# Kernel tuning notes

Measured on AMD Instinct MI355X. Metric: run time of the kernel, lower is better.

## Reference

```python
import jax, jax.numpy as jnp
import numpy as np

N, E, F, ED, H, L, O = 100000, 600000, 64, 16, 128, 4, 32


def _ln(x, g, b, eps=1e-5):
    mu = jnp.mean(x, axis=-1, keepdims=True)
    var = jnp.mean((x - mu) ** 2, axis=-1, keepdims=True)
    return (x - mu) / jnp.sqrt(var + eps) * g + b


def setup_inputs() -> dict:
    key = jax.random.key(0)
    ks = iter(jax.random.split(key, 40))
    s = 0.05
    rn = lambda *shape: jax.random.normal(next(ks), shape, dtype=jnp.float32) * s
    inp = {
        'node_features': jax.random.normal(next(ks), (N, F), dtype=jnp.float32),
        'edge_index': jax.random.randint(next(ks), (2, E), 0, N, dtype=jnp.int64),
        'edge_features': jax.random.normal(next(ks), (E, ED), dtype=jnp.float32),
        # CircuitEncoder: Linear(F,H) -> ReLU -> LayerNorm(H) -> Linear(H,H) -> ReLU
        'enc_w1': rn(F, H), 'enc_b1': jnp.zeros((H,), jnp.float32),
        'enc_ln_g': jnp.ones((H,), jnp.float32), 'enc_ln_b': jnp.zeros((H,), jnp.float32),
        'enc_w2': rn(H, H), 'enc_b2': jnp.zeros((H,), jnp.float32),
        # L stacked GNN layers
        'msg_w1': rn(L, 2 * H + ED, H), 'msg_b1': jnp.zeros((L, H), jnp.float32),
        'msg_w2': rn(L, H, H), 'msg_b2': jnp.zeros((L, H), jnp.float32),
        'upd_w': rn(L, 2 * H, H), 'upd_b': jnp.zeros((L, H), jnp.float32),
        'ln_g': jnp.ones((L, H), jnp.float32), 'ln_b': jnp.zeros((L, H), jnp.float32),
        # GlobalAttentionPool: Linear(H,H//2) -> Tanh -> Linear(H//2,1)
        'att_w1': rn(H, H // 2), 'att_b1': jnp.zeros((H // 2,), jnp.float32),
        'att_w2': rn(H // 2, 1), 'att_b2': jnp.zeros((1,), jnp.float32),
        # output head (dropout is eval-mode identity)
        'head_w1': rn(H, H), 'head_b1': jnp.zeros((H,), jnp.float32),
        'head_w2': rn(H, O), 'head_b2': jnp.zeros((O,), jnp.float32),
    }
    return inp


def reference(node_features, edge_index, edge_features,
              enc_w1, enc_b1, enc_ln_g, enc_ln_b, enc_w2, enc_b2,
              msg_w1, msg_b1, msg_w2, msg_b2, upd_w, upd_b, ln_g, ln_b,
              att_w1, att_b1, att_w2, att_b2,
              head_w1, head_b1, head_w2, head_b2):
    # node encoder
    h = jax.nn.relu(node_features @ enc_w1 + enc_b1)
    h = _ln(h, enc_ln_g, enc_ln_b)
    h = jax.nn.relu(h @ enc_w2 + enc_b2)

    src, dst = edge_index[0], edge_index[1]
    ones_e = jnp.ones((E, 1), h.dtype)
    counts = jax.ops.segment_sum(ones_e, dst, num_segments=N)  # [N,1]
    inv_cnt = 1.0 / (counts + 1e-8)

    for i in range(L):
        # gather -> concat -> message MLP  [E, 2H+ED] -> [E, H]
        m_in = jnp.concatenate([h[src], h[dst], edge_features], axis=-1)
        m = jax.nn.relu(m_in @ msg_w1[i] + msg_b1[i]) @ msg_w2[i] + msg_b2[i]
        # scatter-mean aggregate
        agg = jax.ops.segment_sum(m, dst, num_segments=N) * inv_cnt
        h_new = jax.nn.relu(jnp.concatenate([h, agg], axis=-1) @ upd_w[i] + upd_b[i])
        h = _ln(h + h_new, ln_g[i], ln_b[i])

    # global attention pool (softmax over nodes, dim 0)
    scores = jnp.tanh(h @ att_w1 + att_b1) @ att_w2 + att_b2  # [N,1]
    attn = jax.nn.softmax(scores, axis=0)
    g = jnp.sum(attn * h, axis=0)  # [H]

    # output head (dropout = identity in eval)
    out = jax.nn.relu(g @ head_w1 + head_b1) @ head_w2 + head_b2  # [O]
    return out
```

## Files before the change

### kernel.cpp

```cpp
#include <hip/hip_runtime.h>
#include <hip/hip_bf16.h>

#define NN 100000
#define EE 600000
#define FF 64
#define EDIM 16
#define HH 128
#define LLAYERS 4
#define OO 32

#define SCH 512
#define SNB ((NN + SCH - 1) / SCH)


__global__ __launch_bounds__(64) void k_detect(const unsigned int* __restrict__ w,
                                               int* __restrict__ flag)
{
  const int t = threadIdx.x;
  int z = (w[2*t + 1] == 0u) ? 1 : 0;
  #pragma unroll
  for (int o = 32; o > 0; o >>= 1) z &= __shfl_xor(z, o, 64);
  if (t == 0) *flag = z;
}

__global__ __launch_bounds__(256) void k_cnt(const void* __restrict__ buf,
                                             const int* __restrict__ flag,
                                             float* __restrict__ cnt)
{
  const int is64 = *flag;
  const long long* b64 = (const long long*)buf;
  const int*       b32 = (const int*)buf;
  for (int e = blockIdx.x*256 + threadIdx.x; e < EE; e += gridDim.x*256) {
    const int d = is64 ? (int)b64[EE + e] : b32[EE + e];
    atomicAdd(&cnt[d], 1.0f);
  }
}

__global__ __launch_bounds__(256) void k_scan_a(const float* __restrict__ cnt,
                                                int* __restrict__ bsum)
{
  __shared__ int red[4];
  const int base = blockIdx.x * SCH;
  const int t = threadIdx.x;
  int s = 0;
  const int i0 = base + t, i1 = base + 256 + t;
  if (i0 < NN) s += (int)cnt[i0];
  if (i1 < NN) s += (int)cnt[i1];
  #pragma unroll
  for (int o = 32; o > 0; o >>= 1) s += __shfl_xor(s, o, 64);
  if ((t & 63) == 0) red[t >> 6] = s;
  __syncthreads();
  if (t == 0) bsum[blockIdx.x] = red[0] + red[1] + red[2] + red[3];
}

__global__ __launch_bounds__(256) void k_scan_b(int* __restrict__ bsum)
{
  __shared__ int ps[256];
  const int t = threadIdx.x;
  const int v = (t < SNB) ? bsum[t] : 0;
  ps[t] = v;
  __syncthreads();
  for (int off = 1; off < 256; off <<= 1) {
    int u = (t >= off) ? ps[t - off] : 0;
    __syncthreads();
    ps[t] += u;
    __syncthreads();
  }
  if (t < SNB) bsum[t] = ps[t] - v;
}

__global__ __launch_bounds__(256) void k_scan_c(const float* __restrict__ cnt,
                                                const int* __restrict__ bsum,
                                                int* __restrict__ rowoff,
                                                int* __restrict__ cursor)
{
  __shared__ int vals[SCH];
  __shared__ int ps[256];
  const int base = blockIdx.x * SCH;
  const int t = threadIdx.x;
  const int i0 = base + t, i1 = base + 256 + t;
  vals[t]       = (i0 < NN) ? (int)cnt[i0] : 0;
  vals[256 + t] = (i1 < NN) ? (int)cnt[i1] : 0;
  __syncthreads();
  const int a = vals[2*t], b = vals[2*t + 1];
  const int pair = a + b;
  ps[t] = pair;
  __syncthreads();
  for (int off = 1; off < 256; off <<= 1) {
    int u = (t >= off) ? ps[t - off] : 0;
    __syncthreads();
    ps[t] += u;
    __syncthreads();
  }
  const int excl = bsum[blockIdx.x] + ps[t] - pair;
  const int j0 = base + 2*t, j1 = j0 + 1;
  if (j0 < NN) { rowoff[j0] = excl;     cursor[j0] = excl; }
  if (j1 < NN) { rowoff[j1] = excl + a; cursor[j1] = excl + a; }
  if (j1 == NN - 1) rowoff[NN] = excl + pair;
}

__global__ __launch_bounds__(256) void k_scatter(const void* __restrict__ buf,
                                                 const int* __restrict__ flag,
                                                 int* __restrict__ cursor,
                                                 int* __restrict__ src_perm,
                                                 int* __restrict__ eid_perm)
{
  const int is64 = *flag;
  const long long* b64 = (const long long*)buf;
  const int*       b32 = (const int*)buf;
  for (int e = blockIdx.x*256 + threadIdx.x; e < EE; e += gridDim.x*256) {
    const int s = is64 ? (int)b64[e]      : b32[e];
    const int d = is64 ? (int)b64[EE + e] : b32[EE + e];
    const int pos = atomicAdd(&cursor[d], 1);
    src_perm[pos] = s;
    eid_perm[pos] = e;
  }
}

__global__ __launch_bounds__(256) void k_enc(
    const float* __restrict__ nf, const float* __restrict__ w1,
    const float* __restrict__ b1, const float* __restrict__ lng,
    const float* __restrict__ lnb, const float* __restrict__ w2,
    const float* __restrict__ b2, float* __restrict__ h)
{
  __shared__ float lds[4096];
  __shared__ float red[8];
  const int t = threadIdx.x;
  const int col = t & 127, g = t >> 7;
  float br1[64], br2[128];
  const float4* w14 = (const float4*)w1;
  #pragma unroll
  for (int c = 0; c < 2; ++c) {
    #pragma unroll
    for (int v = 0; v < 4; ++v) ((float4*)lds)[t + v*256] = w14[c*1024 + t + v*256];
    __syncthreads();
    #pragma unroll
    for (int k = 0; k < 32; ++k) br1[c*32+k] = lds[k*128 + col];
    __syncthreads();
  }
  const float4* w24 = (const float4*)w2;
  #pragma unroll
  for (int c = 0; c < 4; ++c) {
    #pragma unroll
    for (int v = 0; v < 4; ++v) ((float4*)lds)[t + v*256] = w24[c*1024 + t + v*256];
    __syncthreads();
    #pragma unroll
    for (int k = 0; k < 32; ++k) br2[c*32+k] = lds[k*128 + col];
    __syncthreads();
  }
  const float b1c = b1[col], gc = lng[col], bc = lnb[col], b2c = b2[col];
  float* xs = lds;
  float* ys = lds + 128;
  for (int n0 = blockIdx.x * 2; n0 < NN; n0 += gridDim.x * 2) {
    const int node = n0 + g;
    if (col < 16) ((float4*)xs)[g*16 + col] = ((const float4*)nf)[(size_t)node*16 + col];
    __syncthreads();
    float a = b1c;
    #pragma unroll
    for (int k = 0; k < 64; ++k) a = fmaf(xs[g*64+k], br1[k], a);
    float v = fmaxf(a, 0.f);
    float s1 = v, s2 = v*v;
    #pragma unroll
    for (int o = 32; o > 0; o >>= 1) { s1 += __shfl_xor(s1, o, 64); s2 += __shfl_xor(s2, o, 64); }
    const int w = (t >> 6) & 1;
    if ((t & 63) == 0) { red[(g*2+w)*2] = s1; red[(g*2+w)*2+1] = s2; }
    __syncthreads();
    const float sum1 = red[g*4] + red[g*4+2], sum2 = red[g*4+1] + red[g*4+3];
    const float mu = sum1 * (1.f/128.f);
    const float var = sum2 * (1.f/128.f) - mu*mu;
    const float y = (v - mu) * rsqrtf(var + 1e-5f) * gc + bc;
    ys[g*128+col] = y;
    __syncthreads();
    float a2 = b2c;
    #pragma unroll
    for (int k = 0; k < 128; ++k) a2 = fmaf(ys[g*128+k], br2[k], a2);
    h[(size_t)node*128 + col] = fmaxf(a2, 0.f);
    __syncthreads();
  }
}

__global__ __launch_bounds__(256) void k_pq(
    const float* __restrict__ h, const float* __restrict__ W1,
    float* __restrict__ PQ)
{
  __shared__ float lds[4096];
  const int t = threadIdx.x;
  const int col = t & 127, hb = t >> 7;
  float br[128];
  const float4* B4 = (const float4*)W1;
  #pragma unroll
  for (int c = 0; c < 8; ++c) {
    #pragma unroll
    for (int v = 0; v < 4; ++v) ((float4*)lds)[t + v*256] = B4[c*1024 + t + v*256];
    __syncthreads();
    if ((c >> 2) == hb) {
      #pragma unroll
      for (int k = 0; k < 32; ++k) br[(c&3)*32 + k] = lds[k*128 + col];
    }
    __syncthreads();
  }
  float4* hs4 = (float4*)lds;
  for (int n0 = blockIdx.x*4; n0 < NN; n0 += gridDim.x*4) {
    if (t < 128) hs4[t] = ((const float4*)h)[(size_t)n0*32 + t];
    __syncthreads();
    float ac[4] = {0.f,0.f,0.f,0.f};
    #pragma unroll
    for (int kq = 0; kq < 32; ++kq) {
      const float b0 = br[4*kq], b1_ = br[4*kq+1], b2_ = br[4*kq+2], b3_ = br[4*kq+3];
      #pragma unroll
      for (int j = 0; j < 4; ++j) {
        float4 a = hs4[j*32 + kq];
        ac[j] = fmaf(a.x,b0, fmaf(a.y,b1_, fmaf(a.z,b2_, fmaf(a.w,b3_, ac[j]))));
      }
    }
    #pragma unroll
    for (int j = 0; j < 4; ++j) PQ[(size_t)(n0+j)*256 + t] = ac[j];
    __syncthreads();
  }
}

__global__ __launch_bounds__(256) void k_edge_csr(
    const int* __restrict__ rowoff, const int* __restrict__ src_perm,
    const int* __restrict__ eid_perm, const float* __restrict__ ef,
    const float* __restrict__ PQ, const float* __restrict__ W1c,
    const float* __restrict__ b1, float* __restrict__ S)
{
  const int t = threadIdx.x;
  const int lane = t & 63, wid = t >> 6;
  float wr0[16], wr1[16];
  #pragma unroll
  for (int k = 0; k < 16; ++k) {
    wr0[k] = W1c[k*128 + lane];
    wr1[k] = W1c[k*128 + 64 + lane];
  }
  const float b1c0 = b1[lane], b1c1 = b1[64+lane];
  const int nwaves = gridDim.x * 4;
  for (int n = blockIdx.x*4 + wid; n < NN; n += nwaves) {
    const int jb = rowoff[n], je = rowoff[n+1];
    const float* Qp = PQ + (size_t)n*256 + 128;
    const float q0 = Qp[lane], q1 = Qp[64+lane];
    float acc0 = 0.f, acc1 = 0.f;
    for (int j = jb; j < je; ++j) {
      const int s   = __builtin_amdgcn_readfirstlane(src_perm[j]);
      const int eid = __builtin_amdgcn_readfirstlane(eid_perm[j]);
      const float4* ef4 = (const float4*)(ef + (size_t)eid*16);
      float4 f0 = ef4[0], f1 = ef4[1], f2 = ef4[2], f3 = ef4[3];
      float fv[16];
      fv[0]=f0.x; fv[1]=f0.y; fv[2]=f0.z; fv[3]=f0.w;
      fv[4]=f1.x; fv[5]=f1.y; fv[6]=f1.z; fv[7]=f1.w;
      fv[8]=f2.x; fv[9]=f2.y; fv[10]=f2.z; fv[11]=f2.w;
      fv[12]=f3.x; fv[13]=f3.y; fv[14]=f3.z; fv[15]=f3.w;
      float r0 = b1c0, r1 = b1c1;
      #pragma unroll
      for (int k = 0; k < 16; ++k) { r0 = fmaf(fv[k], wr0[k], r0); r1 = fmaf(fv[k], wr1[k], r1); }
      const float* Pp = PQ + (size_t)s*256;
      acc0 += fmaxf(r0 + Pp[lane]    + q0, 0.f);
      acc1 += fmaxf(r1 + Pp[64+lane] + q1, 0.f);
    }
    float* Sp = S + (size_t)n*128;
    Sp[lane]      = acc0;
    Sp[64 + lane] = acc1;
  }
}

__global__ __launch_bounds__(256) void k_tagg(
    float* __restrict__ S, const float* __restrict__ W2)
{
  __shared__ float lds[4096];
  const int t = threadIdx.x, col = t & 127, g = t >> 7;
  float br[128];
  const float4* B4 = (const float4*)W2;
  #pragma unroll
  for (int c = 0; c < 4; ++c) {
    #pragma unroll
    for (int v = 0; v < 4; ++v) ((float4*)lds)[t + v*256] = B4[c*1024 + t + v*256];
    __syncthreads();
    #pragma unroll
    for (int k = 0; k < 32; ++k) br[c*32+k] = lds[k*128 + col];
    __syncthreads();
  }
  float4* ss4 = (float4*)lds;
  for (int n0 = blockIdx.x*8; n0 < NN; n0 += gridDim.x*8) {
    ss4[t] = ((const float4*)S)[(size_t)n0*32 + t];
    __syncthreads();
    float ac[4] = {0.f,0.f,0.f,0.f};
    const int rb = g*128;
    #pragma unroll
    for (int kq = 0; kq < 32; ++kq) {
      const float b0 = br[4*kq], b1_ = br[4*kq+1], b2_ = br[4*kq+2], b3_ = br[4*kq+3];
      #pragma unroll
      for (int j = 0; j < 4; ++j) {
        float4 a = ss4[rb + j*32 + kq];
        ac[j] = fmaf(a.x,b0, fmaf(a.y,b1_, fmaf(a.z,b2_, fmaf(a.w,b3_, ac[j]))));
      }
    }
    #pragma unroll
    for (int j = 0; j < 4; ++j) S[(size_t)(n0 + g*4 + j)*128 + col] = ac[j];
    __syncthreads();
  }
}

__global__ __launch_bounds__(256) void k_update(
    float* __restrict__ h, const float* __restrict__ T,
    const float* __restrict__ cnt, const float* __restrict__ U,
    const float* __restrict__ ub, const float* __restrict__ b2,
    const float* __restrict__ lg, const float* __restrict__ lb)
{
  __shared__ float lds[1024];
  __shared__ float bst[4096];
  __shared__ float red[16];
  const int t = threadIdx.x, col = t & 127, hb = t >> 7;
  float br[128];
  const float4* B4 = (const float4*)U;
  #pragma unroll
  for (int c = 0; c < 8; ++c) {
    #pragma unroll
    for (int v = 0; v < 4; ++v) ((float4*)bst)[t + v*256] = B4[c*1024 + t + v*256];
    __syncthreads();
    if ((c >> 2) == hb) {
      #pragma unroll
      for (int k = 0; k < 32; ++k) br[(c&3)*32 + k] = bst[k*128 + col];
    }
    __syncthreads();
  }
  const float ubc = ub[col], lgc = lg[col], lbc = lb[col];
  float* hs = lds; float* as = lds + 512; float* ps = bst;
  for (int n0 = blockIdx.x*4; n0 < NN; n0 += gridDim.x*4) {
    if (hb == 0) {
      ((float4*)hs)[t] = ((const float4*)h)[(size_t)n0*32 + t];
    } else {
      const int tt = t & 127;
      const int j = tt >> 5, k4 = tt & 31;
      const float c_ = cnt[n0 + j];
      const float inv = 1.f / (c_ + 1e-8f);
      float4 tv = ((const float4*)T)[(size_t)n0*32 + tt];
      float4 bv = ((const float4*)b2)[k4];
      float4 av;
      av.x = (tv.x + c_*bv.x)*inv; av.y = (tv.y + c_*bv.y)*inv;
      av.z = (tv.z + c_*bv.z)*inv; av.w = (tv.w + c_*bv.w)*inv;
      ((float4*)as)[tt] = av;
    }
    __syncthreads();
    const float4* A4 = (const float4*)(hb ? as : hs);
    float ac[4] = {0.f,0.f,0.f,0.f};
    #pragma unroll
    for (int kq = 0; kq < 32; ++kq) {
      const float b0 = br[4*kq], b1_ = br[4*kq+1], b2_ = br[4*kq+2], b3_ = br[4*kq+3];
      #pragma unroll
      for (int j = 0; j < 4; ++j) {
        float4 a = A4[j*32 + kq];
        ac[j] = fmaf(a.x,b0, fmaf(a.y,b1_, fmaf(a.z,b2_, fmaf(a.w,b3_, ac[j]))));
      }
    }
    if (hb == 1) {
      #pragma unroll
      for (int j = 0; j < 4; ++j) ps[j*128 + col] = ac[j];
    }
    __syncthreads();
    float rs[4], s1[4], s2[4];
    #pragma unroll
    for (int j = 0; j < 4; ++j) {
      float tot = ac[j] + ps[j*128 + col] + ubc;
      rs[j] = hs[j*128 + col] + fmaxf(tot, 0.f);
      s1[j] = rs[j]; s2[j] = rs[j]*rs[j];
    }
    #pragma unroll
    for (int o = 32; o > 0; o >>= 1) {
      #pragma unroll
      for (int j = 0; j < 4; ++j) {
        s1[j] += __shfl_xor(s1[j], o, 64);
        s2[j] += __shfl_xor(s2[j], o, 64);
      }
    }
    const int w = (t >> 6) & 1;
    if (t < 128 && (t & 63) == 0) {
      #pragma unroll
      for (int j = 0; j < 4; ++j) { red[(j*2+w)*2] = s1[j]; red[(j*2+w)*2+1] = s2[j]; }
    }
    __syncthreads();
    if (t < 128) {
      #pragma unroll
      for (int j = 0; j < 4; ++j) {
        const float sum1 = red[j*4] + red[j*4+2], sum2 = red[j*4+1] + red[j*4+3];
        const float mu = sum1 * (1.f/128.f);
        const float var = sum2 * (1.f/128.f) - mu*mu;
        h[(size_t)(n0+j)*128 + col] = (rs[j]-mu)*rsqrtf(var+1e-5f)*lgc + lbc;
      }
    }
    __syncthreads();
  }
}

__global__ __launch_bounds__(256) void k_score(
    const float* __restrict__ h, const float* __restrict__ aw1,
    const float* __restrict__ ab1, const float* __restrict__ aw2,
    const float* __restrict__ ab2, float* __restrict__ sco)
{
  __shared__ float lds[4096];
  const int t = threadIdx.x, lane = t & 63, wid = t >> 6;
  float br[128];
  const float4* B4 = (const float4*)aw1;
  #pragma unroll
  for (int c = 0; c < 2; ++c) {
    #pragma unroll
    for (int v = 0; v < 4; ++v) ((float4*)lds)[t + v*256] = B4[c*1024 + t + v*256];
    __syncthreads();
    #pragma unroll
    for (int k = 0; k < 64; ++k) br[c*64+k] = lds[k*64 + lane];
    __syncthreads();
  }
  const float b1c = ab1[lane], w2c = aw2[lane], b2c = ab2[0];
  float4* hs4 = (float4*)lds;
  for (int n0 = blockIdx.x*4; n0 < NN; n0 += gridDim.x*4) {
    if (t < 128) hs4[t] = ((const float4*)h)[(size_t)n0*32 + t];
    __syncthreads();
    float p0=0.f, p1=0.f, p2=0.f, p3=0.f;
    #pragma unroll
    for (int kq = 0; kq < 32; ++kq) {
      float4 a = hs4[wid*32 + kq];
      p0 = fmaf(a.x, br[4*kq],   p0);
      p1 = fmaf(a.y, br[4*kq+1], p1);
      p2 = fmaf(a.z, br[4*kq+2], p2);
      p3 = fmaf(a.w, br[4*kq+3], p3);
    }
    float t1 = tanhf(p0+p1+p2+p3 + b1c) * w2c;
    #pragma unroll
    for (int o = 32; o > 0; o >>= 1) t1 += __shfl_xor(t1, o, 64);
    if (lane == 0) sco[n0 + wid] = t1 + b2c;
    __syncthreads();
  }
}

__global__ __launch_bounds__(256) void k_rmax1(const float* __restrict__ sco,
                                               float* __restrict__ pmax)
{
  __shared__ float red[4];
  float m = -1e30f;
  for (int i = blockIdx.x*256 + threadIdx.x; i < NN; i += gridDim.x*256)
    m = fmaxf(m, sco[i]);
  #pragma unroll
  for (int o = 32; o > 0; o >>= 1) m = fmaxf(m, __shfl_xor(m, o, 64));
  if ((threadIdx.x & 63) == 0) red[threadIdx.x >> 6] = m;
  __syncthreads();
  if (threadIdx.x == 0)
    pmax[blockIdx.x] = fmaxf(fmaxf(red[0],red[1]), fmaxf(red[2],red[3]));
}

__global__ __launch_bounds__(256) void k_rmax2(const float* __restrict__ pmax,
                                               float* __restrict__ aux)
{
  __shared__ float red[4];
  float m = pmax[threadIdx.x];
  #pragma unroll
  for (int o = 32; o > 0; o >>= 1) m = fmaxf(m, __shfl_xor(m, o, 64));
  if ((threadIdx.x & 63) == 0) red[threadIdx.x >> 6] = m;
  __syncthreads();
  if (threadIdx.x == 0) {
    aux[0] = fmaxf(fmaxf(red[0],red[1]), fmaxf(red[2],red[3]));
    aux[1] = 0.f;
  }
  if (threadIdx.x < 128) aux[2 + threadIdx.x] = 0.f;
}

__global__ __launch_bounds__(256) void k_pool(
    const float* __restrict__ h, const float* __restrict__ sco,
    float* __restrict__ aux)
{
  __shared__ float ps[256];
  __shared__ float wsum[2];
  const int t = threadIdx.x, col = t & 127, g = t >> 7;
  const float gmax = aux[0];
  float acc = 0.f, wacc = 0.f;
  for (int n0 = blockIdx.x*2; n0 < NN; n0 += gridDim.x*2) {
    const int n = n0 + g;
    const float w = expf(sco[n] - gmax);
    acc = fmaf(w, h[(size_t)n*128 + col], acc);
    if (col == 0) wacc += w;
  }
  ps[t] = acc;
  if (col == 0) wsum[g] = wacc;
  __syncthreads();
  if (t < 128) atomicAdd(&aux[2 + t], ps[t] + ps[128 + t]);
  if (t == 0)  atomicAdd(&aux[1], wsum[0] + wsum[1]);
}

__global__ __launch_bounds__(256) void k_head(
    const float* __restrict__ aux, const float* __restrict__ hw1,
    const float* __restrict__ hb1, const float* __restrict__ hw2,
    const float* __restrict__ hb2, float* __restrict__ out)
{
  __shared__ float gs[128], hsm[128];
  const int t = threadIdx.x;
  if (t < 128) gs[t] = aux[2+t] / aux[1];
  __syncthreads();
  if (t < 128) {
    float a = hb1[t];
    #pragma unroll 4
    for (int k = 0; k < 128; ++k) a = fmaf(gs[k], hw1[k*128 + t], a);
    hsm[t] = fmaxf(a, 0.f);
  }
  __syncthreads();
  if (t < 32) {
    float a = hb2[t];
    #pragma unroll 4
    for (int k = 0; k < 128; ++k) a = fmaf(hsm[k], hw2[k*32 + t], a);
    out[t] = a;
  }
}

extern "C" void kernel_launch(void* const* d_in, const int* in_sizes, int n_in,
                              void* d_out, int out_size, void* d_ws, size_t ws_size,
                              hipStream_t stream)
{
  const float* nf   = (const float*)d_in[0];
  const void*  eraw = d_in[1];
  const float* ef   = (const float*)d_in[2];
  const float* ew1  = (const float*)d_in[3];
  const float* eb1  = (const float*)d_in[4];
  const float* elng = (const float*)d_in[5];
  const float* elnb = (const float*)d_in[6];
  const float* ew2  = (const float*)d_in[7];
  const float* eb2  = (const float*)d_in[8];
  const float* mw1  = (const float*)d_in[9];
  const float* mb1  = (const float*)d_in[10];
  const float* mw2  = (const float*)d_in[11];
  const float* mb2  = (const float*)d_in[12];
  const float* uw   = (const float*)d_in[13];
  const float* ubb  = (const float*)d_in[14];
  const float* lng  = (const float*)d_in[15];
  const float* lnb  = (const float*)d_in[16];
  const float* aw1  = (const float*)d_in[17];
  const float* ab1  = (const float*)d_in[18];
  const float* aw2  = (const float*)d_in[19];
  const float* ab2  = (const float*)d_in[20];
  const float* hw1  = (const float*)d_in[21];
  const float* hb1  = (const float*)d_in[22];
  const float* hw2  = (const float*)d_in[23];
  const float* hb2  = (const float*)d_in[24];

  float* ws   = (float*)d_ws;
  float* h    = ws;
  float* PQ   = ws + (size_t)NN*HH;
  float* S    = ws + (size_t)NN*HH*3;
  float* cnt  = ws + (size_t)NN*HH*4;
  float* sco  = cnt + NN;
  float* pmax = sco + NN;
  float* aux  = pmax + 256;
  int*   flag   = (int*)(aux + 130);
  int*   rowoff = flag + 2;
  int*   cursor = rowoff + NN + 1;
  int*   srcp   = cursor + NN;
  int*   eidp   = srcp + EE;
  int*   bsum   = eidp + EE;

  hipMemsetAsync(cnt, 0, NN*sizeof(float), stream);
  k_detect<<<1, 64, 0, stream>>>((const unsigned int*)eraw, flag);
  k_cnt<<<1024, 256, 0, stream>>>(eraw, flag, cnt);
  k_scan_a<<<SNB, 256, 0, stream>>>(cnt, bsum);
  k_scan_b<<<1, 256, 0, stream>>>(bsum);
  k_scan_c<<<SNB, 256, 0, stream>>>(cnt, bsum, rowoff, cursor);
  k_scatter<<<1024, 256, 0, stream>>>(eraw, flag, cursor, srcp, eidp);
  k_enc<<<1024, 256, 0, stream>>>(nf, ew1, eb1, elng, elnb, ew2, eb2, h);

  for (int i = 0; i < LLAYERS; ++i) {
    k_pq<<<1024, 256, 0, stream>>>(h, mw1 + (size_t)i*272*128, PQ);
    k_edge_csr<<<2048, 256, 0, stream>>>(rowoff, srcp, eidp, ef, PQ,
                                         mw1 + ((size_t)i*272 + 256)*128,
                                         mb1 + (size_t)i*128, S);
    k_tagg<<<1024, 256, 0, stream>>>(S, mw2 + (size_t)i*128*128);
    k_update<<<1024, 256, 0, stream>>>(h, S, cnt,
                                       uw  + (size_t)i*256*128,
                                       ubb + (size_t)i*128,
                                       mb2 + (size_t)i*128,
                                       lng + (size_t)i*128,
                                       lnb + (size_t)i*128);
  }

  k_score<<<512, 256, 0, stream>>>(h, aw1, ab1, aw2, ab2, sco);
  k_rmax1<<<256, 256, 0, stream>>>(sco, pmax);
  k_rmax2<<<1, 256, 0, stream>>>(pmax, aux);
  k_pool<<<256, 256, 0, stream>>>(h, sco, aux);
  k_head<<<1, 256, 0, stream>>>(aux, hw1, hb1, hw2, hb2, (float*)d_out);
}
```

Baseline: 2.514 ms.

## Fold message W2 into update weights to eliminate per-node aggregate transform kernel

Precomputes V = W2·U_agg and w = b2·U_agg per layer in a small prep kernel, so the update kernel multiplies the raw aggregated hidden sums S by V directly. The bias term is handled per node via cnt. This removes the separate k_tagg pass, which read and wrote the full N×H buffer and did a 128×128 matmul per node in every layer. The cost is a small one-time prep kernel and a slightly different floating-point summation order.

```diff
diff --git a/kernel.cpp b/kernel.cpp
--- a/kernel.cpp
+++ b/kernel.cpp
@@ -1,5 +1,6 @@
 #include <hip/hip_runtime.h>
 #include <hip/hip_bf16.h>
+#include <stdint.h>
 
 #define NN 100000
 #define EE 600000
@@ -114,6 +115,42 @@
     const int pos = atomicAdd(&cursor[d], 1);
     src_perm[pos] = s;
     eid_perm[pos] = e;
+  }
+}
+
+__global__ __launch_bounds__(256) void k_prep(
+    const float* __restrict__ mw2, const float* __restrict__ mb2,
+    const float* __restrict__ uw, float* __restrict__ V,
+    float* __restrict__ wv)
+{
+  __shared__ float w2s[16*128];
+  const int L = blockIdx.x >> 3, sub = blockIdx.x & 7;
+  const int t = threadIdx.x, col = t & 127, half = t >> 7;
+  const float* W2 = mw2 + (size_t)L*128*128;
+  const float* Ub = uw  + (size_t)L*256*128 + 128*128;
+  const float* b2 = mb2 + (size_t)L*128;
+  float* Vl = V  + (size_t)L*128*128;
+  float* wl = wv + (size_t)L*128;
+  const float4* W24 = (const float4*)W2;
+  ((float4*)w2s)[t]       = W24[sub*512 + t];
+  ((float4*)w2s)[256 + t] = W24[sub*512 + 256 + t];
+  float ur[128];
+  #pragma unroll 8
+  for (int k = 0; k < 128; ++k) ur[k] = Ub[k*128 + col];
+  __syncthreads();
+  #pragma unroll
+  for (int i = 0; i < 8; ++i) {
+    const int r = half*8 + i;
+    float acc = 0.f;
+    #pragma unroll 8
+    for (int k = 0; k < 128; ++k) acc = fmaf(w2s[r*128 + k], ur[k], acc);
+    Vl[(size_t)(sub*16 + r)*128 + col] = acc;
+  }
+  if (sub == 0 && half == 0) {
+    float acc = 0.f;
+    #pragma unroll 8
+    for (int k = 0; k < 128; ++k) acc = fmaf(b2[k], ur[k], acc);
+    wl[col] = acc;
   }
 }
 
@@ -263,82 +300,50 @@
   }
 }
 
-__global__ __launch_bounds__(256) void k_tagg(
-    float* __restrict__ S, const float* __restrict__ W2)
-{
-  __shared__ float lds[4096];
-  const int t = threadIdx.x, col = t & 127, g = t >> 7;
-  float br[128];
-  const float4* B4 = (const float4*)W2;
-  #pragma unroll
-  for (int c = 0; c < 4; ++c) {
-    #pragma unroll
-    for (int v = 0; v < 4; ++v) ((float4*)lds)[t + v*256] = B4[c*1024 + t + v*256];
-    __syncthreads();
-    #pragma unroll
-    for (int k = 0; k < 32; ++k) br[c*32+k] = lds[k*128 + col];
-    __syncthreads();
-  }
-  float4* ss4 = (float4*)lds;
-  for (int n0 = blockIdx.x*8; n0 < NN; n0 += gridDim.x*8) {
-    ss4[t] = ((const float4*)S)[(size_t)n0*32 + t];
-    __syncthreads();
-    float ac[4] = {0.f,0.f,0.f,0.f};
-    const int rb = g*128;
-    #pragma unroll
-    for (int kq = 0; kq < 32; ++kq) {
-      const float b0 = br[4*kq], b1_ = br[4*kq+1], b2_ = br[4*kq+2], b3_ = br[4*kq+3];
-      #pragma unroll
-      for (int j = 0; j < 4; ++j) {
-        float4 a = ss4[rb + j*32 + kq];
-        ac[j] = fmaf(a.x,b0, fmaf(a.y,b1_, fmaf(a.z,b2_, fmaf(a.w,b3_, ac[j]))));
-      }
-    }
-    #pragma unroll
-    for (int j = 0; j < 4; ++j) S[(size_t)(n0 + g*4 + j)*128 + col] = ac[j];
-    __syncthreads();
-  }
-}
-
-__global__ __launch_bounds__(256) void k_update(
-    float* __restrict__ h, const float* __restrict__ T,
+__global__ __launch_bounds__(256) void k_update2(
+    float* __restrict__ h, const float* __restrict__ S,
     const float* __restrict__ cnt, const float* __restrict__ U,
-    const float* __restrict__ ub, const float* __restrict__ b2,
-    const float* __restrict__ lg, const float* __restrict__ lb)
+    const float* __restrict__ Vl, const float* __restrict__ wv,
+    const float* __restrict__ ub, const float* __restrict__ lg,
+    const float* __restrict__ lb)
 {
   __shared__ float lds[1024];
   __shared__ float bst[4096];
   __shared__ float red[16];
   const int t = threadIdx.x, col = t & 127, hb = t >> 7;
   float br[128];
-  const float4* B4 = (const float4*)U;
-  #pragma unroll
-  for (int c = 0; c < 8; ++c) {
-    #pragma unroll
-    for (int v = 0; v < 4; ++v) ((float4*)bst)[t + v*256] = B4[c*1024 + t + v*256];
-    __syncthreads();
-    if ((c >> 2) == hb) {
-      #pragma unroll
-      for (int k = 0; k < 32; ++k) br[(c&3)*32 + k] = bst[k*128 + col];
-    }
-    __syncthreads();
-  }
-  const float ubc = ub[col], lgc = lg[col], lbc = lb[col];
+  const float4* U4 = (const float4*)U;
+  #pragma unroll
+  for (int c = 0; c < 4; ++c) {
+    #pragma unroll
+    for (int v = 0; v < 4; ++v) ((float4*)bst)[t + v*256] = U4[c*1024 + t + v*256];
+    __syncthreads();
+    if (hb == 0) {
+      #pragma unroll
+      for (int k = 0; k < 32; ++k) br[c*32 + k] = bst[k*128 + col];
+    }
+    __syncthreads();
+  }
+  const float4* V4 = (const float4*)Vl;
+  #pragma unroll
+  for (int c = 0; c < 4; ++c) {
+    #pragma unroll
+    for (int v = 0; v < 4; ++v) ((float4*)bst)[t + v*256] = V4[c*1024 + t + v*256];
+    __syncthreads();
+    if (hb == 1) {
+      #pragma unroll
+      for (int k = 0; k < 32; ++k) br[c*32 + k] = bst[k*128 + col];
+    }
+    __syncthreads();
+  }
+  const float ubc = ub[col], lgc = lg[col], lbc = lb[col], wc = wv[col];
   float* hs = lds; float* as = lds + 512; float* ps = bst;
   for (int n0 = blockIdx.x*4; n0 < NN; n0 += gridDim.x*4) {
     if (hb == 0) {
       ((float4*)hs)[t] = ((const float4*)h)[(size_t)n0*32 + t];
     } else {
       const int tt = t & 127;
-      const int j = tt >> 5, k4 = tt & 31;
-      const float c_ = cnt[n0 + j];
-      const float inv = 1.f / (c_ + 1e-8f);
-      float4 tv = ((const float4*)T)[(size_t)n0*32 + tt];
-      float4 bv = ((const float4*)b2)[k4];
-      float4 av;
-      av.x = (tv.x + c_*bv.x)*inv; av.y = (tv.y + c_*bv.y)*inv;
-      av.z = (tv.z + c_*bv.z)*inv; av.w = (tv.w + c_*bv.w)*inv;
-      ((float4*)as)[tt] = av;
+      ((float4*)as)[tt] = ((const float4*)S)[(size_t)n0*32 + tt];
     }
     __syncthreads();
     const float4* A4 = (const float4*)(hb ? as : hs);
@@ -360,7 +365,9 @@
     float rs[4], s1[4], s2[4];
     #pragma unroll
     for (int j = 0; j < 4; ++j) {
-      float tot = ac[j] + ps[j*128 + col] + ubc;
+      const float cj = cnt[n0 + j];
+      const float invj = 1.f / (cj + 1e-8f);
+      float tot = ac[j] + invj*(ps[j*128 + col] + cj*wc) + ubc;
       rs[j] = hs[j*128 + col] + fmaxf(tot, 0.f);
       s1[j] = rs[j]; s2[j] = rs[j]*rs[j];
     }
@@ -552,6 +559,8 @@
   int*   srcp   = cursor + NN;
   int*   eidp   = srcp + EE;
   int*   bsum   = eidp + EE;
+  float* V  = (float*)(((uintptr_t)(bsum + SNB) + 15) & ~(uintptr_t)15);
+  float* wv = V + (size_t)LLAYERS*HH*HH;
 
   hipMemsetAsync(cnt, 0, NN*sizeof(float), stream);
   k_detect<<<1, 64, 0, stream>>>((const unsigned int*)eraw, flag);
@@ -560,6 +569,7 @@
   k_scan_b<<<1, 256, 0, stream>>>(bsum);
   k_scan_c<<<SNB, 256, 0, stream>>>(cnt, bsum, rowoff, cursor);
   k_scatter<<<1024, 256, 0, stream>>>(eraw, flag, cursor, srcp, eidp);
+  k_prep<<<LLAYERS*8, 256, 0, stream>>>(mw2, mb2, uw, V, wv);
   k_enc<<<1024, 256, 0, stream>>>(nf, ew1, eb1, elng, elnb, ew2, eb2, h);
 
   for (int i = 0; i < LLAYERS; ++i) {
@@ -567,13 +577,13 @@
     k_edge_csr<<<2048, 256, 0, stream>>>(rowoff, srcp, eidp, ef, PQ,
                                          mw1 + ((size_t)i*272 + 256)*128,
                                          mb1 + (size_t)i*128, S);
-    k_tagg<<<1024, 256, 0, stream>>>(S, mw2 + (size_t)i*128*128);
-    k_update<<<1024, 256, 0, stream>>>(h, S, cnt,
-                                       uw  + (size_t)i*256*128,
-                                       ubb + (size_t)i*128,
-                                       mb2 + (size_t)i*128,
-                                       lng + (size_t)i*128,
-                                       lnb + (size_t)i*128);
+    k_update2<<<1024, 256, 0, stream>>>(h, S, cnt,
+                                        uw + (size_t)i*256*128,
+                                        V  + (size_t)i*HH*HH,
+                                        wv + (size_t)i*HH,
+                                        ubb + (size_t)i*128,
+                                        lng + (size_t)i*128,
+                                        lnb + (size_t)i*128);
   }
 
   k_score<<<512, 256, 0, stream>>>(h, aw1, ab1, aw2, ab2, sco);
```

Result: slower. 2.752 ms (+9.5%).
